# Kernel optimization log

Hardware: AMD Instinct MI355X
Metric: run time of the kernel (lower is better)

## Reference

```python
import jax, jax.numpy as jnp
import numpy as np

B, T, C_IN, H, W = 4096, 256, 16, 1, 1
HID, NCLS = 64, 10


def setup_inputs() -> dict:
    key = jax.random.key(0)
    ks = jax.random.split(key, 8)
    s = 0.1
    x = jax.random.normal(ks[0], (B, T, C_IN, H, W), dtype=jnp.float32)
    # ConvLSTM cell: 1x1 conv over concat([x_t, h]) -> 4*HID gate channels
    W_lstm = jax.random.normal(ks[1], (4 * HID, C_IN + HID), dtype=jnp.float32) * s
    b_lstm = jnp.zeros((4 * HID,), dtype=jnp.float32)
    W_class = jax.random.normal(ks[2], (NCLS, HID), dtype=jnp.float32) * s
    b_class = jnp.zeros((NCLS,), dtype=jnp.float32)
    W_dec = jax.random.normal(ks[3], (1, HID), dtype=jnp.float32) * s
    b_dec = jnp.zeros((1,), dtype=jnp.float32)
    return {"x": x, "W_lstm": W_lstm, "b_lstm": b_lstm,
            "W_class": W_class, "b_class": b_class,
            "W_dec": W_dec, "b_dec": b_dec}


def _conv1x1(z, Wm, bv):
    # 1x1 conv == channel contraction; z: [B,C,H,W], Wm: [O,C]
    return jnp.einsum('bchw,oc->bohw', z, Wm) + bv[None, :, None, None]


def reference(x, W_lstm, b_lstm, W_class, b_class, W_dec, b_dec):
    Bn, Tn, Cn, Hn, Wn = x.shape
    hid = W_class.shape[1]
    h0 = jnp.zeros((Bn, hid, Hn, Wn), dtype=x.dtype)
    c0 = jnp.zeros((Bn, hid, Hn, Wn), dtype=x.dtype)
    pnd0 = jnp.ones((Bn, Hn, Wn), dtype=x.dtype)  # proba_not_decided_yet

    def step(carry, xt):
        h, c, pnd = carry
        comb = jnp.concatenate([xt, h], axis=1)
        gates = _conv1x1(comb, W_lstm, b_lstm)
        i, f, o, g = jnp.split(gates, 4, axis=1)
        c_next = jax.nn.sigmoid(f) * c + jax.nn.sigmoid(i) * jnp.tanh(g)
        h_next = jax.nn.sigmoid(o) * jnp.tanh(c_next)
        dec = jax.nn.sigmoid(_conv1x1(h_next, W_dec, b_dec))[:, 0]  # [B,H,W]
        logp = jax.nn.log_softmax(_conv1x1(h_next, W_class, b_class), axis=1)
        pnd_next = pnd * (1.0 - dec)
        return (h_next, c_next, pnd_next), (logp, dec, pnd)

    xt_seq = jnp.moveaxis(x, 1, 0)  # [T,B,C,H,W]
    _, (logps, decs, pnds) = jax.lax.scan(step, (h0, c0, pnd0), xt_seq)
    logps = jnp.moveaxis(logps, 0, 1)  # [B,T,NCLS,H,W]
    decs = jnp.moveaxis(decs, 0, 1)    # [B,T,H,W]
    pnds = jnp.moveaxis(pnds, 0, 1)    # pnd BEFORE step t
    is_last = (jnp.arange(Tn) == Tn - 1)[None, :, None, None]
    # Pt = dec_t * pnd_t for t < T-1 ; Pt = pnd_{T-1} at the last step
    Pts = jnp.where(is_last, pnds, decs * pnds)
    return logps, Pts
```

## Files before the change

kernel.cpp:

```cpp
#include <hip/hip_runtime.h>
#include <hip/hip_bf16.h>

#define Bsz  4096
#define Tn   256
#define CIN  16
#define NCLS 10
#define MB   16

typedef __attribute__((ext_vector_type(8))) short short8;
typedef __attribute__((ext_vector_type(4))) float f32x4;

#if __has_builtin(__builtin_amdgcn_exp2f)
#define EXP2F(x) __builtin_amdgcn_exp2f(x)
#else
#define EXP2F(x) exp2f(x)
#endif
#define RCPF(x) __builtin_amdgcn_rcpf(x)

#define LOG2E 1.442695041f

__device__ inline ushort f2bf(float f) {
    union { float f; unsigned u; } x; x.f = f;
    return (ushort)((x.u + 0x7FFF + ((x.u >> 16) & 1)) >> 16);
}

__global__ __launch_bounds__(512, 2) void dualrnn_kernel(
    const float* __restrict__ x,  const float* __restrict__ Wl, const float* __restrict__ bl,
    const float* __restrict__ Wc, const float* __restrict__ bc,
    const float* __restrict__ Wd, const float* __restrict__ bd,
    float* __restrict__ out)
{
    __shared__ alignas(16) ushort comb[2][16][104];
    const int tid  = threadIdx.x;
    const int wave = tid >> 6;
    const int lane = tid & 63;
    const int col  = lane & 15;
    const int grp  = lane >> 4;
    const int b0   = blockIdx.x * MB;
    const bool gatew = (wave < 4);

    for (int i = tid; i < 2 * 16 * 104; i += 512) ((ushort*)comb)[i] = 0;

    short8 wf[4][3]; f32x4 biasv[4];
    short8 wcd[2];   f32x4 bcdv;
    if (gatew) {
#pragma unroll
        for (int g = 0; g < 4; ++g) {
            const float sc = (g == 3) ? 2.f * LOG2E : -LOG2E;
            const int R = g * 64 + wave * 16 + col;
            const float bv = bl[R] * sc;
            biasv[g] = (f32x4){bv, bv, bv, bv};
#pragma unroll
            for (int kt = 0; kt < 3; ++kt)
#pragma unroll
                for (int i = 0; i < 8; ++i) {
                    const int k = kt * 32 + grp * 8 + i;
                    wf[g][kt][i] = (short)f2bf(k < 80 ? Wl[R * 80 + k] * sc : 0.f);
                }
        }
    } else {
#pragma unroll
        for (int kt = 0; kt < 2; ++kt)
#pragma unroll
            for (int i = 0; i < 8; ++i) {
                const int k = kt * 32 + grp * 8 + i;
                float v = 0.f;
                if (col < 10)       v = Wc[col * 64 + k];
                else if (col == 10) v = Wd[k] * -LOG2E;
                wcd[kt][i] = (short)f2bf(v);
            }
        const float bv = (col < 10) ? bc[col] : ((col == 10) ? bd[0] * -LOG2E : 0.f);
        bcdv = (f32x4){bv, bv, bv, bv};
    }

    __syncthreads();

    if (tid < 256) {
        const int r = tid >> 4, ch = tid & 15;
        comb[0][r][ch] = f2bf(x[((size_t)(b0 + r) * Tn) * CIN + ch]);
    }
    __syncthreads();

    float cst[4] = {0, 0, 0, 0};
    float pnd = 1.f;

    const int hw  = wave & 3;
    const int row = grp * 4 + hw;
    float* lp_p = out + ((size_t)(b0 + row) * Tn) * NCLS + col;
    float* pt_p = out + (size_t)Bsz * Tn * NCLS + (size_t)(b0 + row) * Tn;
    const int t2 = hw * 64 + lane;
    const int xr = t2 >> 4, xc = t2 & 15;
    float xva = 0.f;
    const float* xp = x + ((size_t)(b0 + xr) * Tn + 2) * CIN + xc;
    if (!gatew) xva = x[((size_t)(b0 + xr) * Tn + 1) * CIN + xc];

    for (int t = 0; t < Tn; ++t) {
        const ushort (*rdb)[104] = comb[t & 1];
        ushort (*wrb)[104] = comb[(t + 1) & 1];
        if (gatew) {
            const short8 a0 = *(const short8*)&rdb[col][ 0 + grp * 8];
            const short8 a1 = *(const short8*)&rdb[col][32 + grp * 8];
            const short8 a2 = *(const short8*)&rdb[col][64 + grp * 8];
            f32x4 acc[4];
#pragma unroll
            for (int g = 0; g < 4; ++g) {
                f32x4 z = biasv[g];
                z = __builtin_amdgcn_mfma_f32_16x16x32_bf16(a0, wf[g][0], z, 0, 0, 0);
                z = __builtin_amdgcn_mfma_f32_16x16x32_bf16(a1, wf[g][1], z, 0, 0, 0);
                z = __builtin_amdgcn_mfma_f32_16x16x32_bf16(a2, wf[g][2], z, 0, 0, 0);
                acc[g] = z;
            }
            const int hc = 16 + wave * 16 + col;
#pragma unroll
            for (int j = 0; j < 4; ++j) {
                const float ei = EXP2F(acc[0][j]);
                const float ef = EXP2F(acc[1][j]);
                const float eo = EXP2F(acc[2][j]);
                const float eg = EXP2F(acc[3][j]);
                const float A  = 1.f + ei, Bv = 1.f + ef;
                const float G1 = eg + 1.f, G2 = eg - 1.f, O = 1.f + eo;
                const float t0  = A * G1;
                const float num = cst[j] * t0 + G2 * Bv;
                const float den = Bv * t0;
                const float cn  = num * RCPF(den);
                cst[j] = cn;
                const float e2 = EXP2F(2.f * LOG2E * cn);
                const float h  = (e2 - 1.f) * RCPF((e2 + 1.f) * O);
                wrb[grp * 4 + j][hc] = f2bf(h);
            }
        } else {
            float xvn = 0.f;
            if (t + 2 < Tn) xvn = *xp;
            xp += CIN;
            const short8 ha0 = *(const short8*)&rdb[col][16 + grp * 8];
            const short8 ha1 = *(const short8*)&rdb[col][48 + grp * 8];
            f32x4 cz = bcdv;
            cz = __builtin_amdgcn_mfma_f32_16x16x32_bf16(ha0, wcd[0], cz, 0, 0, 0);
            cz = __builtin_amdgcn_mfma_f32_16x16x32_bf16(ha1, wcd[1], cz, 0, 0, 0);
            if (t + 1 < Tn) wrb[xr][xc] = f2bf(xva);
            xva = xvn;
            if (t > 0) {
                float v = (hw & 1) ? ((hw & 2) ? cz[3] : cz[1])
                                   : ((hw & 2) ? cz[2] : cz[0]);
                float s = (col < 10) ? EXP2F(v * LOG2E) : 0.f;
                s += __int_as_float(__builtin_amdgcn_ds_swizzle(__float_as_int(s), 0x041F));
                s += __int_as_float(__builtin_amdgcn_ds_swizzle(__float_as_int(s), 0x081F));
                s += __int_as_float(__builtin_amdgcn_ds_swizzle(__float_as_int(s), 0x101F));
                s += __int_as_float(__builtin_amdgcn_ds_swizzle(__float_as_int(s), 0x201F));
                const float lse = __logf(s);
                if (col < 10) {
                    lp_p[0] = v - lse;
                } else if (col == 10) {
                    const float d = RCPF(1.f + EXP2F(v));
                    pt_p[0] = d * pnd;
                    pnd *= (1.f - d);
                }
                lp_p += NCLS;
                pt_p += 1;
            }
        }
        __syncthreads();
    }

    if (!gatew) {
        const ushort (*rdb)[104] = comb[Tn & 1];
        const short8 ha0 = *(const short8*)&rdb[col][16 + grp * 8];
        const short8 ha1 = *(const short8*)&rdb[col][48 + grp * 8];
        f32x4 cz = bcdv;
        cz = __builtin_amdgcn_mfma_f32_16x16x32_bf16(ha0, wcd[0], cz, 0, 0, 0);
        cz = __builtin_amdgcn_mfma_f32_16x16x32_bf16(ha1, wcd[1], cz, 0, 0, 0);
        float v = (hw & 1) ? ((hw & 2) ? cz[3] : cz[1])
                           : ((hw & 2) ? cz[2] : cz[0]);
        float s = (col < 10) ? EXP2F(v * LOG2E) : 0.f;
        s += __int_as_float(__builtin_amdgcn_ds_swizzle(__float_as_int(s), 0x041F));
        s += __int_as_float(__builtin_amdgcn_ds_swizzle(__float_as_int(s), 0x081F));
        s += __int_as_float(__builtin_amdgcn_ds_swizzle(__float_as_int(s), 0x101F));
        s += __int_as_float(__builtin_amdgcn_ds_swizzle(__float_as_int(s), 0x201F));
        const float lse = __logf(s);
        if (col < 10)       lp_p[0] = v - lse;
        else if (col == 10) pt_p[0] = pnd;
    }
}

extern "C" void kernel_launch(void* const* d_in, const int* in_sizes, int n_in,
                              void* d_out, int out_size, void* d_ws, size_t ws_size,
                              hipStream_t stream) {
    const float* x  = (const float*)d_in[0];
    const float* Wl = (const float*)d_in[1];
    const float* bl = (const float*)d_in[2];
    const float* Wc = (const float*)d_in[3];
    const float* bc = (const float*)d_in[4];
    const float* Wd = (const float*)d_in[5];
    const float* bd = (const float*)d_in[6];
    float* out = (float*)d_out;

    dim3 grid(Bsz / MB), block(512);
    hipLaunchKernelGGL(dualrnn_kernel, grid, block, 0, stream,
                       x, Wl, bl, Wc, bc, Wd, bd, out);
}
```

Before: 150.2 us.

## Duplicate gate MFMAs across 8 waves and split elementwise LSTM update by row half

Raises the block from 512 to 768 threads and uses 8 gate waves instead of 4. Each pair of waves computes the same gate MFMAs but handles only half of the accumulator rows in the sigmoid/tanh cell update, which shortens the serial transcendental chain per step. It also raises wave priority around the MFMA issue. The cost is duplicated MFMA work, more registers and waves per block, and a larger barrier group each timestep.

```diff
diff --git a/kernel.cpp b/kernel.cpp
--- a/kernel.cpp
+++ b/kernel.cpp
@@ -24,7 +24,7 @@
     return (ushort)((x.u + 0x7FFF + ((x.u >> 16) & 1)) >> 16);
 }
 
-__global__ __launch_bounds__(512, 2) void dualrnn_kernel(
+__global__ __launch_bounds__(768, 3) void dualrnn_kernel(
     const float* __restrict__ x,  const float* __restrict__ Wl, const float* __restrict__ bl,
     const float* __restrict__ Wc, const float* __restrict__ bc,
     const float* __restrict__ Wd, const float* __restrict__ bd,
@@ -37,17 +37,19 @@
     const int col  = lane & 15;
     const int grp  = lane >> 4;
     const int b0   = blockIdx.x * MB;
-    const bool gatew = (wave < 4);
-
-    for (int i = tid; i < 2 * 16 * 104; i += 512) ((ushort*)comb)[i] = 0;
+    const bool gatew = (wave < 8);
+
+    for (int i = tid; i < 2 * 16 * 104; i += 768) ((ushort*)comb)[i] = 0;
 
     short8 wf[4][3]; f32x4 biasv[4];
     short8 wcd[2];   f32x4 bcdv;
+    const int ub = wave & 3;
+    const int jh = (wave >> 2) & 1;
     if (gatew) {
 #pragma unroll
         for (int g = 0; g < 4; ++g) {
             const float sc = (g == 3) ? 2.f * LOG2E : -LOG2E;
-            const int R = g * 64 + wave * 16 + col;
+            const int R = g * 64 + ub * 16 + col;
             const float bv = bl[R] * sc;
             biasv[g] = (f32x4){bv, bv, bv, bv};
 #pragma unroll
@@ -81,7 +83,7 @@
     }
     __syncthreads();
 
-    float cst[4] = {0, 0, 0, 0};
+    float cst[2] = {0, 0};
     float pnd = 1.f;
 
     const int hw  = wave & 3;
@@ -101,6 +103,7 @@
             const short8 a0 = *(const short8*)&rdb[col][ 0 + grp * 8];
             const short8 a1 = *(const short8*)&rdb[col][32 + grp * 8];
             const short8 a2 = *(const short8*)&rdb[col][64 + grp * 8];
+            __builtin_amdgcn_s_setprio(1);
             f32x4 acc[4];
 #pragma unroll
             for (int g = 0; g < 4; ++g) {
@@ -110,23 +113,28 @@
                 z = __builtin_amdgcn_mfma_f32_16x16x32_bf16(a2, wf[g][2], z, 0, 0, 0);
                 acc[g] = z;
             }
-            const int hc = 16 + wave * 16 + col;
-#pragma unroll
-            for (int j = 0; j < 4; ++j) {
-                const float ei = EXP2F(acc[0][j]);
-                const float ef = EXP2F(acc[1][j]);
-                const float eo = EXP2F(acc[2][j]);
-                const float eg = EXP2F(acc[3][j]);
+            __builtin_amdgcn_s_setprio(0);
+            const int hc = 16 + ub * 16 + col;
+#pragma unroll
+            for (int jj = 0; jj < 2; ++jj) {
+                const float av_i = jh ? acc[0][jj + 2] : acc[0][jj];
+                const float av_f = jh ? acc[1][jj + 2] : acc[1][jj];
+                const float av_o = jh ? acc[2][jj + 2] : acc[2][jj];
+                const float av_g = jh ? acc[3][jj + 2] : acc[3][jj];
+                const float ei = EXP2F(av_i);
+                const float ef = EXP2F(av_f);
+                const float eo = EXP2F(av_o);
+                const float eg = EXP2F(av_g);
                 const float A  = 1.f + ei, Bv = 1.f + ef;
                 const float G1 = eg + 1.f, G2 = eg - 1.f, O = 1.f + eo;
                 const float t0  = A * G1;
-                const float num = cst[j] * t0 + G2 * Bv;
+                const float num = cst[jj] * t0 + G2 * Bv;
                 const float den = Bv * t0;
                 const float cn  = num * RCPF(den);
-                cst[j] = cn;
+                cst[jj] = cn;
                 const float e2 = EXP2F(2.f * LOG2E * cn);
                 const float h  = (e2 - 1.f) * RCPF((e2 + 1.f) * O);
-                wrb[grp * 4 + j][hc] = f2bf(h);
+                wrb[grp * 4 + jh * 2 + jj][hc] = f2bf(h);
             }
         } else {
             float xvn = 0.f;
@@ -194,7 +202,7 @@
     const float* bd = (const float*)d_in[6];
     float* out = (float*)d_out;
 
-    dim3 grid(Bsz / MB), block(512);
+    dim3 grid(Bsz / MB), block(768);
     hipLaunchKernelGGL(dualrnn_kernel, grid, block, 0, stream,
                        x, Wl, bl, Wc, bc, Wd, bd, out);
 }
```

Result: slower. 177.1 us (+17.9%).

## Split recurrence from softmax/decision head into separate kernels via workspace

Applied to the files above, without the earlier changes.

Moves the log-softmax and the decision-probability cumulative product out of the recurrent loop. The new 256-thread recurrent kernel computes the gates and the class/decision logits in the same waves and writes the raw logits to a workspace. A parallel head kernel then does the softmax and sigmoid, and a small transposing kernel runs the pnd scan. The aim is to shorten the serial per-step critical path and drop the cross-wave specialisation, at the cost of extra global traffic of about 12 floats per step plus two extra launches. If the workspace is too small it falls back to the fused kernel.

```diff
diff --git a/kernel.cpp b/kernel.cpp
--- a/kernel.cpp
+++ b/kernel.cpp
@@ -24,7 +24,184 @@
     return (ushort)((x.u + 0x7FFF + ((x.u >> 16) & 1)) >> 16);
 }
 
-__global__ __launch_bounds__(512, 2) void dualrnn_kernel(
+__global__ __launch_bounds__(256, 1) void rec_kernel(
+    const float* __restrict__ x,  const float* __restrict__ Wl, const float* __restrict__ bl,
+    const float* __restrict__ Wc, const float* __restrict__ bc,
+    const float* __restrict__ Wd, const float* __restrict__ bd,
+    float* __restrict__ wslog)
+{
+    __shared__ alignas(16) ushort comb[2][16][104];
+    const int tid  = threadIdx.x;
+    const int ub   = tid >> 6;
+    const int lane = tid & 63;
+    const int col  = lane & 15;
+    const int grp  = lane >> 4;
+    const int b0   = blockIdx.x * MB;
+
+    for (int i = tid; i < 2 * 16 * 104; i += 256) ((ushort*)comb)[i] = 0;
+
+    short8 wf[4][3]; f32x4 biasv[4];
+#pragma unroll
+    for (int g = 0; g < 4; ++g) {
+        const float sc = (g == 3) ? 2.f * LOG2E : -LOG2E;
+        const int R = g * 64 + ub * 16 + col;
+        const float bv = bl[R] * sc;
+        biasv[g] = (f32x4){bv, bv, bv, bv};
+#pragma unroll
+        for (int kt = 0; kt < 3; ++kt)
+#pragma unroll
+            for (int i = 0; i < 8; ++i) {
+                const int k = kt * 32 + grp * 8 + i;
+                wf[g][kt][i] = (short)f2bf(k < 80 ? Wl[R * 80 + k] * sc : 0.f);
+            }
+    }
+    short8 wcd[2];
+#pragma unroll
+    for (int kt = 0; kt < 2; ++kt)
+#pragma unroll
+        for (int i = 0; i < 8; ++i) {
+            const int k = kt * 32 + grp * 8 + i;
+            float v = 0.f;
+            if (col < 10)       v = Wc[col * 64 + k];
+            else if (col == 10) v = Wd[k];
+            wcd[kt][i] = (short)f2bf(v);
+        }
+    const float bv2 = (col < 10) ? bc[col] : ((col == 10) ? bd[0] : 0.f);
+    const f32x4 bcdv = {bv2, bv2, bv2, bv2};
+
+    __syncthreads();
+    comb[0][tid >> 4][tid & 15] =
+        f2bf(x[((size_t)(b0 + (tid >> 4)) * Tn) * CIN + (tid & 15)]);
+    __syncthreads();
+
+    float cst[4] = {0, 0, 0, 0};
+    const int xr = tid >> 4, xc = tid & 15;
+    float xva = x[((size_t)(b0 + xr) * Tn + 1) * CIN + xc];
+    const float* xp = x + ((size_t)(b0 + xr) * Tn + 2) * CIN + xc;
+
+    const int orow = grp * 4 + ub;
+    float* lgp = wslog + ((size_t)(b0 + orow) * Tn) * 12 + col;
+
+    for (int t = 0; t < Tn; ++t) {
+        const ushort (*rdb)[104] = comb[t & 1];
+        ushort (*wrb)[104] = comb[(t + 1) & 1];
+        float xvn = 0.f;
+        if (t + 2 < Tn) xvn = *xp;
+        xp += CIN;
+        const short8 a0  = *(const short8*)&rdb[col][ 0 + grp * 8];
+        const short8 a1  = *(const short8*)&rdb[col][32 + grp * 8];
+        const short8 a2  = *(const short8*)&rdb[col][64 + grp * 8];
+        const short8 ha0 = *(const short8*)&rdb[col][16 + grp * 8];
+        const short8 ha1 = *(const short8*)&rdb[col][48 + grp * 8];
+
+        f32x4 acc[4];
+#pragma unroll
+        for (int g = 0; g < 4; ++g) {
+            f32x4 z = biasv[g];
+            z = __builtin_amdgcn_mfma_f32_16x16x32_bf16(a0, wf[g][0], z, 0, 0, 0);
+            z = __builtin_amdgcn_mfma_f32_16x16x32_bf16(a1, wf[g][1], z, 0, 0, 0);
+            z = __builtin_amdgcn_mfma_f32_16x16x32_bf16(a2, wf[g][2], z, 0, 0, 0);
+            acc[g] = z;
+        }
+        f32x4 cz = bcdv;
+        cz = __builtin_amdgcn_mfma_f32_16x16x32_bf16(ha0, wcd[0], cz, 0, 0, 0);
+        cz = __builtin_amdgcn_mfma_f32_16x16x32_bf16(ha1, wcd[1], cz, 0, 0, 0);
+
+        const int hc = 16 + ub * 16 + col;
+#pragma unroll
+        for (int j = 0; j < 4; ++j) {
+            const float ei = EXP2F(acc[0][j]);
+            const float ef = EXP2F(acc[1][j]);
+            const float eo = EXP2F(acc[2][j]);
+            const float eg = EXP2F(acc[3][j]);
+            const float A  = 1.f + ei, Bv = 1.f + ef;
+            const float G1 = eg + 1.f, G2 = eg - 1.f, O = 1.f + eo;
+            const float t0  = A * G1;
+            const float num = cst[j] * t0 + G2 * Bv;
+            const float den = Bv * t0;
+            const float cn  = num * RCPF(den);
+            cst[j] = cn;
+            const float e2 = EXP2F(2.f * LOG2E * cn);
+            const float h  = (e2 - 1.f) * RCPF((e2 + 1.f) * O);
+            wrb[grp * 4 + j][hc] = f2bf(h);
+        }
+        if (t + 1 < Tn) wrb[xr][xc] = f2bf(xva);
+        xva = xvn;
+        if (t > 0) {
+            if (col < 11) {
+                const float v = (ub == 0) ? cz[0] : (ub == 1) ? cz[1]
+                              : (ub == 2) ? cz[2] : cz[3];
+                lgp[0] = v;
+            }
+            lgp += 12;
+        }
+        __syncthreads();
+    }
+    {
+        const ushort (*rdb)[104] = comb[Tn & 1];
+        const short8 ha0 = *(const short8*)&rdb[col][16 + grp * 8];
+        const short8 ha1 = *(const short8*)&rdb[col][48 + grp * 8];
+        f32x4 cz = bcdv;
+        cz = __builtin_amdgcn_mfma_f32_16x16x32_bf16(ha0, wcd[0], cz, 0, 0, 0);
+        cz = __builtin_amdgcn_mfma_f32_16x16x32_bf16(ha1, wcd[1], cz, 0, 0, 0);
+        if (col < 11) {
+            const float v = (ub == 0) ? cz[0] : (ub == 1) ? cz[1]
+                          : (ub == 2) ? cz[2] : cz[3];
+            lgp[0] = v;
+        }
+    }
+}
+
+__global__ __launch_bounds__(256) void head_kernel(
+    const float* __restrict__ wslog, float* __restrict__ out, float* __restrict__ dec)
+{
+    const size_t r = (size_t)blockIdx.x * 256 + threadIdx.x;
+    const float4* lg = (const float4*)(wslog + r * 12);
+    const float4 v0 = lg[0], v1 = lg[1], v2 = lg[2];
+    const float e0 = EXP2F(v0.x * LOG2E), e1 = EXP2F(v0.y * LOG2E);
+    const float e2 = EXP2F(v0.z * LOG2E), e3 = EXP2F(v0.w * LOG2E);
+    const float e4 = EXP2F(v1.x * LOG2E), e5 = EXP2F(v1.y * LOG2E);
+    const float e6 = EXP2F(v1.z * LOG2E), e7 = EXP2F(v1.w * LOG2E);
+    const float e8 = EXP2F(v2.x * LOG2E), e9 = EXP2F(v2.y * LOG2E);
+    const float s = ((e0 + e1) + (e2 + e3)) + ((e4 + e5) + (e6 + e7)) + (e8 + e9);
+    const float lse = __logf(s);
+    float* lp = out + r * 10;
+    ((float2*)lp)[0] = (float2){v0.x - lse, v0.y - lse};
+    ((float2*)lp)[1] = (float2){v0.z - lse, v0.w - lse};
+    ((float2*)lp)[2] = (float2){v1.x - lse, v1.y - lse};
+    ((float2*)lp)[3] = (float2){v1.z - lse, v1.w - lse};
+    ((float2*)lp)[4] = (float2){v2.x - lse, v2.y - lse};
+    dec[r] = RCPF(1.f + EXP2F(-v2.z * LOG2E));
+}
+
+__global__ __launch_bounds__(64) void pnd_kernel(
+    const float* __restrict__ dec, float* __restrict__ pt)
+{
+    __shared__ float tile[64][65];
+    const int ln = threadIdx.x;
+    const int b0 = blockIdx.x * 64;
+    float pnd = 1.f;
+    for (int tc = 0; tc < Tn; tc += 64) {
+#pragma unroll 8
+        for (int i = 0; i < 64; ++i)
+            tile[i][ln] = dec[(size_t)(b0 + i) * Tn + tc + ln];
+        __syncthreads();
+        for (int tl = 0; tl < 64; ++tl) {
+            const float d = tile[ln][tl];
+            float v = d * pnd;
+            if (tc + tl == Tn - 1) v = pnd;
+            tile[ln][tl] = v;
+            pnd *= (1.f - d);
+        }
+        __syncthreads();
+        float* dst = pt + (size_t)(b0 + ln) * Tn + tc;
+#pragma unroll 8
+        for (int k = 0; k < 64; ++k) dst[k] = tile[ln][k];
+        __syncthreads();
+    }
+}
+
+__global__ __launch_bounds__(512, 2) void dualrnn_fused(
     const float* __restrict__ x,  const float* __restrict__ Wl, const float* __restrict__ bl,
     const float* __restrict__ Wc, const float* __restrict__ bc,
     const float* __restrict__ Wd, const float* __restrict__ bd,
@@ -72,9 +249,7 @@
         const float bv = (col < 10) ? bc[col] : ((col == 10) ? bd[0] * -LOG2E : 0.f);
         bcdv = (f32x4){bv, bv, bv, bv};
     }
-
     __syncthreads();
-
     if (tid < 256) {
         const int r = tid >> 4, ch = tid & 15;
         comb[0][r][ch] = f2bf(x[((size_t)(b0 + r) * Tn) * CIN + ch]);
@@ -83,7 +258,6 @@
 
     float cst[4] = {0, 0, 0, 0};
     float pnd = 1.f;
-
     const int hw  = wave & 3;
     const int row = grp * 4 + hw;
     float* lp_p = out + ((size_t)(b0 + row) * Tn) * NCLS + col;
@@ -161,7 +335,6 @@
         }
         __syncthreads();
     }
-
     if (!gatew) {
         const ushort (*rdb)[104] = comb[Tn & 1];
         const short8 ha0 = *(const short8*)&rdb[col][16 + grp * 8];
@@ -194,7 +367,21 @@
     const float* bd = (const float*)d_in[6];
     float* out = (float*)d_out;
 
-    dim3 grid(Bsz / MB), block(512);
-    hipLaunchKernelGGL(dualrnn_kernel, grid, block, 0, stream,
-                       x, Wl, bl, Wc, bc, Wd, bd, out);
-}
+    const size_t logN = (size_t)Bsz * Tn * 12;
+    const size_t decN = (size_t)Bsz * Tn;
+    const size_t need = (logN + decN) * sizeof(float);
+
+    if (ws_size >= need) {
+        float* wslog = (float*)d_ws;
+        float* dec   = wslog + logN;
+        hipLaunchKernelGGL(rec_kernel, dim3(Bsz / MB), dim3(256), 0, stream,
+                           x, Wl, bl, Wc, bc, Wd, bd, wslog);
+        hipLaunchKernelGGL(head_kernel, dim3((Bsz * Tn) / 256), dim3(256), 0, stream,
+                           wslog, out, dec);
+        hipLaunchKernelGGL(pnd_kernel, dim3(Bsz / 64), dim3(64), 0, stream,
+                           dec, out + (size_t)Bsz * Tn * NCLS);
+    } else {
+        hipLaunchKernelGGL(dualrnn_fused, dim3(Bsz / MB), dim3(512), 0, stream,
+                           x, Wl, bl, Wc, bc, Wd, bd, out);
+    }
+}
```

Result: slower. 187.4 us (+24.8%).
